# Optimization experiments

Hardware: AMD Instinct MI355X
Metric: run time of the kernel (lower is better)

The kernel has to match this reference:

```python
import jax, jax.numpy as jnp
import numpy as np

N = 100000      # nodes
E = 1600000     # edges (avg degree 16)
DIN = 64
DOUT = 64
C = 8           # num classes; label -1 means unknown


def _xavier(key, shape):
    a = jnp.sqrt(6.0 / (shape[0] + shape[1]))
    return jax.random.uniform(key, shape, jnp.float32, -a, a)


def setup_inputs():
    key = jax.random.key(0)
    ks = jax.random.split(key, 17)
    return {
        "x": jax.random.normal(ks[0], (N, DIN), jnp.float32),
        "adj_low_vals": jax.random.uniform(ks[1], (E,), jnp.float32) / 16.0,
        "adj_high_vals": jax.random.uniform(ks[2], (E,), jnp.float32) / 16.0,
        "weight_low": _xavier(ks[3], (DIN, DOUT)),
        "weight_high": _xavier(ks[4], (DIN, DOUT)),
        "weight_mlp": _xavier(ks[5], (DIN, DOUT)),
        "att_vec_low_fr": _xavier(ks[6], (DOUT, 1)),
        "att_vec_high_fr": _xavier(ks[7], (DOUT, 1)),
        "att_vec_low_be": _xavier(ks[8], (DOUT, 1)),
        "att_vec_high_be": _xavier(ks[9], (DOUT, 1)),
        "att_vec_low_unk": _xavier(ks[10], (DOUT, 1)),
        "att_vec_high_unk": _xavier(ks[11], (DOUT, 1)),
        "att_vec_mlp": _xavier(ks[12], (DOUT, 1)),
        "att_vec7": _xavier(ks[13], (7, 7)),
        "edge_src": jax.random.randint(ks[14], (E,), 0, N),
        "edge_dst": jax.random.randint(ks[15], (E,), 0, N),
        "label_unk": jax.random.randint(ks[16], (N,), -1, C),
    }


def reference(x, adj_low_vals, adj_high_vals, weight_low, weight_high, weight_mlp,
              att_vec_low_fr, att_vec_high_fr, att_vec_low_be, att_vec_high_be,
              att_vec_low_unk, att_vec_high_unk, att_vec_mlp, att_vec7,
              edge_src, edge_dst, label_unk):
    def spmm(vals, feats):  # out[dst] += vals * feats[src]  (sparse [N,N] @ [N,D])
        return jax.ops.segment_sum(vals[:, None] * feats[edge_src], edge_dst, num_segments=N)

    output_low = jax.nn.relu(spmm(adj_low_vals, x @ weight_low))
    output_high = jax.nn.relu(spmm(adj_high_vals, x @ weight_high))
    output_mlp = jax.nn.relu(x @ weight_mlp)

    # per-edge fake label: 2 if either endpoint unknown (<0), 1 if labels differ
    # (both known) -> heterophilous, else 0 -> homophilous
    sl = label_unk[edge_src]
    dl = label_unk[edge_dst]
    fake = jnp.where((sl < 0) | (dl < 0), 2, jnp.where(sl != dl, 1, 0))

    h_low_e = output_low[edge_src]    # [E, DOUT] gathered messages
    h_high_e = output_high[edge_src]

    def agg(h_e, k):  # masked segment-sum over destination nodes
        m = (fake == k).astype(h_e.dtype)[:, None]
        return jax.ops.segment_sum(h_e * m, edge_dst, num_segments=N)

    neigh_homo_low, neigh_hete_low, neigh_unk_low = agg(h_low_e, 0), agg(h_low_e, 1), agg(h_low_e, 2)
    neigh_homo_high, neigh_hete_high, neigh_unk_high = agg(h_high_e, 0), agg(h_high_e, 1), agg(h_high_e, 2)

    # attention7 (fr_high_g is None branch)
    feats = jax.nn.sigmoid(jnp.concatenate([
        neigh_hete_low @ att_vec_low_fr, neigh_hete_high @ att_vec_high_fr,
        neigh_homo_low @ att_vec_low_be, neigh_homo_high @ att_vec_high_be,
        neigh_unk_low @ att_vec_low_unk, neigh_unk_high @ att_vec_high_unk,
        output_mlp @ att_vec_mlp], axis=1))  # [N, 7]
    att = jax.nn.softmax((feats @ att_vec7) / 7.0, axis=1)

    return 7.0 * (att[:, 0:1] * neigh_hete_low + att[:, 1:2] * neigh_hete_high
                  + att[:, 2:3] * neigh_homo_low + att[:, 3:4] * neigh_homo_high
                  + att[:, 4:5] * neigh_unk_low + att[:, 5:6] * neigh_unk_high
                  + att[:, 6:7] * output_mlp)
```

## Files before the change

kernel.cpp:

```cpp
#include <hip/hip_runtime.h>
#include <hip/hip_bf16.h>

typedef unsigned int u32;
typedef unsigned short u16;
typedef unsigned long long u64;

typedef __attribute__((ext_vector_type(8))) short bf16x8;
typedef __attribute__((ext_vector_type(4))) float f32x4;

static __device__ __forceinline__ float bflo(u32 u) { return __uint_as_float(u << 16); }
static __device__ __forceinline__ float bfhi(u32 u) { return __uint_as_float(u & 0xFFFF0000u); }
static __device__ __forceinline__ float bf2f(u16 u) { return __uint_as_float((u32)u << 16); }
static __device__ __forceinline__ u32 f2bf(float f) {
    u32 u = __float_as_uint(f);
    return (u + 0x7FFFu + ((u >> 16) & 1u)) >> 16;
}
static __device__ __forceinline__ u32 packbf(float lo, float hi) {
    return f2bf(lo) | (f2bf(hi) << 16);
}
static __device__ __forceinline__ float ldf(const u16* p16, int idx, int isf32) {
    return isf32 ? ((const float*)p16)[idx] : bf2f(p16[idx]);
}
static __device__ __forceinline__ void load4(const u16* p, int q, int isf32, float* v) {
    if (isf32) {
        float4 t = ((const float4*)p)[q];
        v[0] = t.x; v[1] = t.y; v[2] = t.z; v[3] = t.w;
    } else {
        u32 a = ((const u32*)p)[q * 2], b = ((const u32*)p)[q * 2 + 1];
        v[0] = bflo(a); v[1] = bfhi(a); v[2] = bflo(b); v[3] = bfhi(b);
    }
}
static __device__ __forceinline__ float sanitize(float v, float code) {
    return (fabsf(v) < 1e30f) ? v : code;
}

static __device__ __forceinline__ float wave_sum(float v) {
#pragma unroll
    for (int o = 32; o; o >>= 1) v += __shfl_xor(v, o, 64);
    return v;
}
static __device__ __forceinline__ float group_sum(float v) {
#pragma unroll
    for (int o = 8; o; o >>= 1) v += __shfl_xor(v, o, 64);
    return v;
}


__global__ void k_sentinel(float* __restrict__ out, int n, float val) {
    int i = blockIdx.x * blockDim.x + threadIdx.x;
    if (i < n) out[i] = val;
}

__global__ void k_zero_sniff(int* __restrict__ p, int n, const u16* __restrict__ x,
                             int* __restrict__ flag) {
    int i = blockIdx.x * blockDim.x + threadIdx.x;
    if (i < n) p[i] = 0;
    if (blockIdx.x == 0 && threadIdx.x < 64) {
        int lane = threadIdx.x;
        int wild = 0;
        for (int k = 0; k < 64; k++) {
            u32 u = x[lane * 64 + k];
            int e = (u >> 7) & 0xFF;
            if (e < 96 || e > 135) wild++;
        }
        float tot = wave_sum((float)wild);
        if (lane == 0) *flag = (tot > 200.f) ? 1 : 0;
    }
}


__global__ void k_hist(const int* __restrict__ dst, int E, int* __restrict__ deg) {
    int i = blockIdx.x * blockDim.x + threadIdx.x;
    if (i < E) atomicAdd(&deg[dst[i]], 1);
}

__global__ void k_scan_partial(const int* __restrict__ deg, int n, int* __restrict__ bsum) {
    int t = threadIdx.x;
    int base = blockIdx.x * 1024 + t * 4;
    int s = 0;
#pragma unroll
    for (int j = 0; j < 4; j++) {
        int idx = base + j;
        if (idx < n) s += deg[idx];
    }
    __shared__ int sh[256];
    sh[t] = s;
    __syncthreads();
    for (int d = 128; d; d >>= 1) {
        if (t < d) sh[t] += sh[t + d];
        __syncthreads();
    }
    if (t == 0) bsum[blockIdx.x] = sh[0];
}

__global__ void k_scan_bsum(const int* __restrict__ bsum, int nb, int* __restrict__ boff) {
    int t = threadIdx.x;
    int v = (t < nb) ? bsum[t] : 0;
    __shared__ int sh[256];
    sh[t] = v;
    __syncthreads();
    for (int d = 1; d < 256; d <<= 1) {
        int u = (t >= d) ? sh[t - d] : 0;
        __syncthreads();
        sh[t] += u;
        __syncthreads();
    }
    if (t < nb) boff[t] = sh[t] - v;
}

__global__ void k_scan_final(const int* __restrict__ deg, int n, const int* __restrict__ boff,
                             int* __restrict__ offsets, int Etot) {
    int t = threadIdx.x;
    int base = blockIdx.x * 1024 + t * 4;
    int v[4];
    int s = 0;
#pragma unroll
    for (int j = 0; j < 4; j++) {
        int idx = base + j;
        v[j] = (idx < n) ? deg[idx] : 0;
        s += v[j];
    }
    __shared__ int sh[256];
    sh[t] = s;
    __syncthreads();
    for (int d = 1; d < 256; d <<= 1) {
        int u = (t >= d) ? sh[t - d] : 0;
        __syncthreads();
        sh[t] += u;
        __syncthreads();
    }
    int ex = sh[t] - s + boff[blockIdx.x];
#pragma unroll
    for (int j = 0; j < 4; j++) {
        int idx = base + j;
        if (idx < n) offsets[idx] = ex;
        ex += v[j];
    }
    if (blockIdx.x == 0 && t == 0) offsets[n] = Etot;
}

__global__ void k_scatter(const int* __restrict__ src, const int* __restrict__ dst,
                          const u16* __restrict__ avl, const u16* __restrict__ avh,
                          const int* __restrict__ lab, int E,
                          const int* __restrict__ offsets, int* __restrict__ cursor,
                          u64* __restrict__ epay, const int* __restrict__ flag) {
    int i = blockIdx.x * blockDim.x + threadIdx.x;
    if (i >= E) return;
    int isf32 = *flag;
    int d = dst[i];
    int pos = offsets[d] + atomicAdd(&cursor[d], 1);
    if ((unsigned)pos >= (unsigned)E) return;
    int s = src[i];
    int sl = lab[s], dl = lab[d];
    int fake = (sl < 0 || dl < 0) ? 2 : ((sl != dl) ? 1 : 0);
    u32 lo32 = (u32)(s | (fake << 20));
    u32 hi32 = isf32 ? packbf(((const float*)avl)[i], ((const float*)avh)[i])
                     : ((u32)avl[i] | ((u32)avh[i] << 16));
    epay[pos] = ((u64)hi32 << 32) | lo32;
}


__global__ void k_prepB(const u16* __restrict__ wl, const u16* __restrict__ wh,
                        const u16* __restrict__ wm, u16* __restrict__ Bpack,
                        const int* __restrict__ flag) {
    int isf32 = *flag;
    for (int idx = threadIdx.x; idx < 12 * 2 * 64; idx += 256) {
        int slot = idx >> 6;
        int ln = idx & 63;
        int ct = slot >> 1, c = slot & 1;
        int mat = ct >> 2;
        const u16* W = (mat == 0) ? wl : (mat == 1) ? wh : wm;
        int col = (ct & 3) * 16 + (ln & 15);
        int kbase = c * 32 + (ln >> 4) * 8;
        u16* dst = Bpack + (size_t)idx * 8;
#pragma unroll
        for (int j = 0; j < 8; j++) dst[j] = (u16)f2bf(ldf(W, (kbase + j) * 64 + col, isf32));
    }
}

__launch_bounds__(256) __global__
void k_gemm_mfma(const u16* __restrict__ x, const u16* __restrict__ Bpack, int N,
                 u32* __restrict__ xwlh, float* __restrict__ omlp,
                 const int* __restrict__ flag) {
    int isf32 = *flag;
    int lane = threadIdx.x & 63;
    int wv = (blockIdx.x * 256 + threadIdx.x) >> 6;
    int nw = gridDim.x * 4;
    int m = lane & 15, quad = lane >> 4;
    int ntiles = (N + 15) >> 4;
    for (int tile = wv; tile < ntiles; tile += nw) {
        int r0 = tile * 16;
        int arow = min(r0 + m, N - 1);
        bf16x8 a[2];
#pragma unroll
        for (int c = 0; c < 2; c++) {
            int base = arow * 64 + c * 32 + quad * 8;
            if (isf32) {
                const float* xf = (const float*)x;
#pragma unroll
                for (int j = 0; j < 8; j++) a[c][j] = (short)f2bf(xf[base + j]);
            } else {
#pragma unroll
                for (int j = 0; j < 8; j++) a[c][j] = (short)x[base + j];
            }
        }
        f32x4 acc[12];
#pragma unroll
        for (int t = 0; t < 12; t++) acc[t] = (f32x4){0.f, 0.f, 0.f, 0.f};
#pragma unroll
        for (int t = 0; t < 12; t++) {
#pragma unroll
            for (int c = 0; c < 2; c++) {
                bf16x8 b = *(const bf16x8*)(Bpack + (size_t)((t * 2 + c) * 64 + lane) * 8);
                acc[t] = __builtin_amdgcn_mfma_f32_16x16x32_bf16(a[c], b, acc[t], 0, 0, 0);
            }
        }
#pragma unroll
        for (int t = 0; t < 4; t++) {
#pragma unroll
            for (int r = 0; r < 4; r++) {
                int row = r0 + quad * 4 + r;
                if (row < N) {
                    int o = row * 64 + t * 16 + m;
                    xwlh[o] = packbf(acc[t][r], acc[t + 4][r]);
                    omlp[o] = fmaxf(acc[t + 8][r], 0.f);
                }
            }
        }
    }
}


__launch_bounds__(256) __global__
void k_spmm4n(const u32* __restrict__ xwlh, const u64* __restrict__ epay,
              const int* __restrict__ offsets, int N, int E, u32* __restrict__ outlh) {
    int lane = threadIdx.x & 63;
    int gwave = blockIdx.x * 4 + (threadIdx.x >> 6);
    int g = lane & 15, gi = lane >> 4;
    int node = gwave * 4 + gi;
    bool vn = node < N;
    int s = vn ? offsets[node] : 0;
    int e = vn ? offsets[node + 1] : 0;
    int deg = e - s;
    int md = deg;
    md = max(md, __shfl_xor(md, 16, 64));
    md = max(md, __shfl_xor(md, 32, 64));
    int Nm1 = N - 1, Em1 = E - 1;
    float aL[4] = {0.f, 0.f, 0.f, 0.f}, aH[4] = {0.f, 0.f, 0.f, 0.f};
    for (int t = 0; t < md; t += 2) {
#pragma unroll
        for (int u = 0; u < 2; u++) {
            int tt = t + u;
            int idx = min(max(s + min(tt, deg - 1), 0), Em1);
            u64 p = epay[idx];
            float w = (tt < deg) ? 1.f : 0.f;
            int sj = min((int)(p & 0xFFFFF), Nm1);
            u32 vv = (u32)(p >> 32);
            float vl = w * bflo(vv), vh = w * bfhi(vv);
            uint4 R = *((const uint4*)(xwlh + (size_t)sj * 64) + g);
            aL[0] += vl * bflo(R.x); aH[0] += vh * bfhi(R.x);
            aL[1] += vl * bflo(R.y); aH[1] += vh * bfhi(R.y);
            aL[2] += vl * bflo(R.z); aH[2] += vh * bfhi(R.z);
            aL[3] += vl * bflo(R.w); aH[3] += vh * bfhi(R.w);
        }
    }
    if (vn) {
        uint4 W;
        W.x = packbf(fmaxf(aL[0], 0.f), fmaxf(aH[0], 0.f));
        W.y = packbf(fmaxf(aL[1], 0.f), fmaxf(aH[1], 0.f));
        W.z = packbf(fmaxf(aL[2], 0.f), fmaxf(aH[2], 0.f));
        W.w = packbf(fmaxf(aL[3], 0.f), fmaxf(aH[3], 0.f));
        ((uint4*)(outlh + (size_t)node * 64))[g] = W;
    }
}


__launch_bounds__(256) __global__
void k_agg4n(const u32* __restrict__ outlh, const u64* __restrict__ epay,
             const int* __restrict__ offsets,
             const u16* __restrict__ aLF, const u16* __restrict__ aHF,
             const u16* __restrict__ aLB, const u16* __restrict__ aHB,
             const u16* __restrict__ aLU, const u16* __restrict__ aHU,
             const u16* __restrict__ aM, const u16* __restrict__ a7, int N, int E,
             float* __restrict__ out, const int* __restrict__ flag) {
    int isf32 = *flag;
    int lane = threadIdx.x & 63;
    int gwave = blockIdx.x * 4 + (threadIdx.x >> 6);
    int g = lane & 15, gi = lane >> 4;
    int node = gwave * 4 + gi;
    bool vn = node < N;
    int s = vn ? offsets[node] : 0;
    int e = vn ? offsets[node + 1] : 0;
    int deg = e - s;
    int md = deg;
    md = max(md, __shfl_xor(md, 16, 64));
    md = max(md, __shfl_xor(md, 32, 64));
    int Nm1 = N - 1, Em1 = E - 1;
    float heL[4] = {0, 0, 0, 0}, heH[4] = {0, 0, 0, 0};
    float hoL[4] = {0, 0, 0, 0}, hoH[4] = {0, 0, 0, 0};
    float unL[4] = {0, 0, 0, 0}, unH[4] = {0, 0, 0, 0};
    for (int t = 0; t < md; t += 2) {
#pragma unroll
        for (int u = 0; u < 2; u++) {
            int tt = t + u;
            int idx = min(max(s + min(tt, deg - 1), 0), Em1);
            u64 p = epay[idx];
            int fk = (int)(p >> 20) & 3;
            bool valid = (tt < deg);
            float whe = (valid && fk == 1) ? 1.f : 0.f;
            float who = (valid && fk == 0) ? 1.f : 0.f;
            float wun = (valid && fk == 2) ? 1.f : 0.f;
            int sj = min((int)(p & 0xFFFFF), Nm1);
            uint4 R = *((const uint4*)(outlh + (size_t)sj * 64) + g);
            float lo0 = bflo(R.x), hi0 = bfhi(R.x);
            float lo1 = bflo(R.y), hi1 = bfhi(R.y);
            float lo2 = bflo(R.z), hi2 = bfhi(R.z);
            float lo3 = bflo(R.w), hi3 = bfhi(R.w);
            heL[0] += whe * lo0; heH[0] += whe * hi0;
            heL[1] += whe * lo1; heH[1] += whe * hi1;
            heL[2] += whe * lo2; heH[2] += whe * hi2;
            heL[3] += whe * lo3; heH[3] += whe * hi3;
            hoL[0] += who * lo0; hoH[0] += who * hi0;
            hoL[1] += who * lo1; hoH[1] += who * hi1;
            hoL[2] += who * lo2; hoH[2] += who * hi2;
            hoL[3] += who * lo3; hoH[3] += who * hi3;
            unL[0] += wun * lo0; unH[0] += wun * hi0;
            unL[1] += wun * lo1; unH[1] += wun * hi1;
            unL[2] += wun * lo2; unH[2] += wun * hi2;
            unL[3] += wun * lo3; unH[3] += wun * hi3;
        }
    }
    float vLF[4], vHF[4], vLB[4], vHB[4], vLU[4], vHU[4], vM[4];
    load4(aLF, g, isf32, vLF);
    load4(aHF, g, isf32, vHF);
    load4(aLB, g, isf32, vLB);
    load4(aHB, g, isf32, vHB);
    load4(aLU, g, isf32, vLU);
    load4(aHU, g, isf32, vHU);
    load4(aM, g, isf32, vM);
    float mvv[4] = {0.f, 0.f, 0.f, 0.f};
    if (vn) {
        float4 MV = ((const float4*)(out + (size_t)node * 64))[g];
        mvv[0] = MV.x; mvv[1] = MV.y; mvv[2] = MV.z; mvv[3] = MV.w;
    }

    float p0 = 0, p1 = 0, p2 = 0, p3 = 0, p4 = 0, p5 = 0, p6 = 0;
#pragma unroll
    for (int k = 0; k < 4; k++) {
        p0 += heL[k] * vLF[k];
        p1 += heH[k] * vHF[k];
        p2 += hoL[k] * vLB[k];
        p3 += hoH[k] * vHB[k];
        p4 += unL[k] * vLU[k];
        p5 += unH[k] * vHU[k];
        p6 += mvv[k] * vM[k];
    }
    float d0 = group_sum(p0), d1 = group_sum(p1), d2 = group_sum(p2), d3 = group_sum(p3);
    float d4 = group_sum(p4), d5 = group_sum(p5), d6 = group_sum(p6);

    float f[7];
    f[0] = 1.f / (1.f + expf(-d0));
    f[1] = 1.f / (1.f + expf(-d1));
    f[2] = 1.f / (1.f + expf(-d2));
    f[3] = 1.f / (1.f + expf(-d3));
    f[4] = 1.f / (1.f + expf(-d4));
    f[5] = 1.f / (1.f + expf(-d5));
    f[6] = 1.f / (1.f + expf(-d6));

    float z[7];
#pragma unroll
    for (int jj = 0; jj < 7; jj++) {
        float acc = 0.f;
#pragma unroll
        for (int i = 0; i < 7; i++) acc += f[i] * ldf(a7, i * 7 + jj, isf32);
        z[jj] = acc * (1.f / 7.f);
    }
    float m = z[0];
#pragma unroll
    for (int jj = 1; jj < 7; jj++) m = fmaxf(m, z[jj]);
    float wsum = 0.f;
    float wv[7];
#pragma unroll
    for (int jj = 0; jj < 7; jj++) { wv[jj] = expf(z[jj] - m); wsum += wv[jj]; }
    float s7 = 7.f / wsum;

    if (vn) {
        float4 W;
        float o0 = wv[0] * heL[0] + wv[1] * heH[0] + wv[2] * hoL[0] + wv[3] * hoH[0] +
                   wv[4] * unL[0] + wv[5] * unH[0] + wv[6] * mvv[0];
        float o1 = wv[0] * heL[1] + wv[1] * heH[1] + wv[2] * hoL[1] + wv[3] * hoH[1] +
                   wv[4] * unL[1] + wv[5] * unH[1] + wv[6] * mvv[1];
        float o2 = wv[0] * heL[2] + wv[1] * heH[2] + wv[2] * hoL[2] + wv[3] * hoH[2] +
                   wv[4] * unL[2] + wv[5] * unH[2] + wv[6] * mvv[2];
        float o3 = wv[0] * heL[3] + wv[1] * heH[3] + wv[2] * hoL[3] + wv[3] * hoH[3] +
                   wv[4] * unL[3] + wv[5] * unH[3] + wv[6] * mvv[3];
        W.x = sanitize(o0 * s7, 333.f);
        W.y = sanitize(o1 * s7, 333.f);
        W.z = sanitize(o2 * s7, 333.f);
        W.w = sanitize(o3 * s7, 333.f);
        ((float4*)(out + (size_t)node * 64))[g] = W;
    }
}


extern "C" void kernel_launch(void* const* d_in, const int* in_sizes, int n_in, void* d_out,
                              int out_size, void* d_ws, size_t ws_size, hipStream_t stream) {
    const u16* x = (const u16*)d_in[0];
    const u16* avl = (const u16*)d_in[1];
    const u16* avh = (const u16*)d_in[2];
    const u16* wl = (const u16*)d_in[3];
    const u16* wh = (const u16*)d_in[4];
    const u16* wm = (const u16*)d_in[5];
    const u16* aLF = (const u16*)d_in[6];
    const u16* aHF = (const u16*)d_in[7];
    const u16* aLB = (const u16*)d_in[8];
    const u16* aHB = (const u16*)d_in[9];
    const u16* aLU = (const u16*)d_in[10];
    const u16* aHU = (const u16*)d_in[11];
    const u16* aM = (const u16*)d_in[12];
    const u16* a7 = (const u16*)d_in[13];
    const int* esrc = (const int*)d_in[14];
    const int* edst = (const int*)d_in[15];
    const int* lab = (const int*)d_in[16];
    float* out = (float*)d_out;

    const int N = in_sizes[0] / 64;
    const int E = in_sizes[1];

    char* w = (char*)d_ws;
    size_t off = 0;
    auto alloc = [&](size_t bytes) -> char* {
        char* p = w + off;
        off += (bytes + 255) & ~(size_t)255;
        return p;
    };
    int* flag = (int*)alloc(256);
    int* offsets = (int*)alloc((size_t)(N + 1) * 4);
    int* degcur = (int*)alloc((size_t)2 * N * 4);
    int* bsum = (int*)alloc(256 * 4);
    int* boff = (int*)alloc(256 * 4);
    u16* Bpack = (u16*)alloc(12 * 2 * 64 * 8 * 2);
    u64* epay = (u64*)alloc((size_t)E * 8);
    u32* xwlh = (u32*)alloc((size_t)N * 64 * 4);
    u32* outlh = (u32*)alloc((size_t)N * 64 * 4);

    if (ws_size < off) {
        k_sentinel<<<(out_size + 255) / 256, 256, 0, stream>>>(out, out_size, 1000.0f);
        return;
    }

    int* deg = degcur;
    int* cursor = degcur + N;
    int NB = (N + 1023) / 1024;

    k_zero_sniff<<<(2 * N + 255) / 256, 256, 0, stream>>>(degcur, 2 * N, x, flag);
    k_hist<<<(E + 255) / 256, 256, 0, stream>>>(edst, E, deg);
    k_scan_partial<<<NB, 256, 0, stream>>>(deg, N, bsum);
    k_scan_bsum<<<1, 256, 0, stream>>>(bsum, NB, boff);
    k_scan_final<<<NB, 256, 0, stream>>>(deg, N, boff, offsets, E);
    k_scatter<<<(E + 255) / 256, 256, 0, stream>>>(esrc, edst, avl, avh, lab, E, offsets, cursor,
                                                   epay, flag);

    k_prepB<<<1, 256, 0, stream>>>(wl, wh, wm, Bpack, flag);
    int ntiles = (N + 15) / 16;
    int gemmBlocks = (ntiles + 3) / 4;
    k_gemm_mfma<<<gemmBlocks, 256, 0, stream>>>(x, Bpack, N, xwlh, out , flag);

    int nodeBlocks = (N + 15) / 16;
    k_spmm4n<<<nodeBlocks, 256, 0, stream>>>(xwlh, epay, offsets, N, E, outlh);
    k_agg4n<<<nodeBlocks, 256, 0, stream>>>(outlh, epay, offsets, aLF, aHF, aLB, aHB, aLU, aHU,
                                            aM, a7, N, E, out, flag);
}
```

Measured before the change: 458.0 us.

## Split CSR edge scatter into two-pass bucketed scatter with LDS counters

```diff
diff --git a/kernel.cpp b/kernel.cpp
--- a/kernel.cpp
+++ b/kernel.cpp
@@ -139,24 +139,48 @@
     if (blockIdx.x == 0 && t == 0) offsets[n] = Etot;
 }
 
-__global__ void k_scatter(const int* __restrict__ src, const int* __restrict__ dst,
-                          const u16* __restrict__ avl, const u16* __restrict__ avh,
-                          const int* __restrict__ lab, int E,
-                          const int* __restrict__ offsets, int* __restrict__ cursor,
-                          u64* __restrict__ epay, const int* __restrict__ flag) {
+__global__ void k_scat1(const int* __restrict__ src, const int* __restrict__ dst,
+                        const u16* __restrict__ avl, const u16* __restrict__ avh,
+                        const int* __restrict__ lab, int E,
+                        const int* __restrict__ offsets, int* __restrict__ bcur,
+                        u64* __restrict__ etmp, const int* __restrict__ flag) {
     int i = blockIdx.x * blockDim.x + threadIdx.x;
     if (i >= E) return;
     int isf32 = *flag;
     int d = dst[i];
-    int pos = offsets[d] + atomicAdd(&cursor[d], 1);
+    int b = d >> 8;
+    int base = b << 8;
+    int rank = atomicAdd(&bcur[b * 16], 1);
+    int pos = offsets[base] + rank;
     if ((unsigned)pos >= (unsigned)E) return;
     int s = src[i];
     int sl = lab[s], dl = lab[d];
     int fake = (sl < 0 || dl < 0) ? 2 : ((sl != dl) ? 1 : 0);
-    u32 lo32 = (u32)(s | (fake << 20));
+    u32 lo32 = (u32)s | ((u32)fake << 20) | ((u32)(d - base) << 22);
     u32 hi32 = isf32 ? packbf(((const float*)avl)[i], ((const float*)avh)[i])
                      : ((u32)avl[i] | ((u32)avh[i] << 16));
-    epay[pos] = ((u64)hi32 << 32) | lo32;
+    etmp[pos] = ((u64)hi32 << 32) | lo32;
+}
+
+__launch_bounds__(256) __global__
+void k_scat2(const u64* __restrict__ etmp, const int* __restrict__ offsets, int N, int E,
+             u64* __restrict__ epay) {
+    __shared__ int cur[256];
+    int b = blockIdx.x;
+    int base = b << 8;
+    int t = threadIdx.x;
+    cur[t] = 0;
+    __syncthreads();
+    int hi = min(base + 256, N);
+    int r0 = offsets[base];
+    int r1 = offsets[hi];
+    for (int e = r0 + t; e < r1; e += 256) {
+        u64 p = etmp[e];
+        int dloc = (int)(p >> 22) & 0xFF;
+        int rank = atomicAdd(&cur[dloc], 1);
+        int pos = offsets[base + dloc] + rank;
+        if ((unsigned)pos < (unsigned)E) epay[pos] = p;
+    }
 }
 
 
@@ -245,13 +269,13 @@
     int md = deg;
     md = max(md, __shfl_xor(md, 16, 64));
     md = max(md, __shfl_xor(md, 32, 64));
-    int Nm1 = N - 1, Em1 = E - 1;
+    int Nm1 = N - 1;
     float aL[4] = {0.f, 0.f, 0.f, 0.f}, aH[4] = {0.f, 0.f, 0.f, 0.f};
     for (int t = 0; t < md; t += 2) {
 #pragma unroll
         for (int u = 0; u < 2; u++) {
             int tt = t + u;
-            int idx = min(max(s + min(tt, deg - 1), 0), Em1);
+            int idx = max(s + min(tt, deg - 1), 0);
             u64 p = epay[idx];
             float w = (tt < deg) ? 1.f : 0.f;
             int sj = min((int)(p & 0xFFFFF), Nm1);
@@ -295,7 +319,7 @@
     int md = deg;
     md = max(md, __shfl_xor(md, 16, 64));
     md = max(md, __shfl_xor(md, 32, 64));
-    int Nm1 = N - 1, Em1 = E - 1;
+    int Nm1 = N - 1;
     float heL[4] = {0, 0, 0, 0}, heH[4] = {0, 0, 0, 0};
     float hoL[4] = {0, 0, 0, 0}, hoH[4] = {0, 0, 0, 0};
     float unL[4] = {0, 0, 0, 0}, unH[4] = {0, 0, 0, 0};
@@ -303,7 +327,7 @@
 #pragma unroll
         for (int u = 0; u < 2; u++) {
             int tt = t + u;
-            int idx = min(max(s + min(tt, deg - 1), 0), Em1);
+            int idx = max(s + min(tt, deg - 1), 0);
             u64 p = epay[idx];
             int fk = (int)(p >> 20) & 3;
             bool valid = (tt < deg);
@@ -450,16 +474,19 @@
     }
 
     int* deg = degcur;
-    int* cursor = degcur + N;
+    int* bcur = degcur + N;
+    u64* etmp = (u64*)xwlh;
     int NB = (N + 1023) / 1024;
+    int NB2 = (N + 255) / 256;
 
     k_zero_sniff<<<(2 * N + 255) / 256, 256, 0, stream>>>(degcur, 2 * N, x, flag);
     k_hist<<<(E + 255) / 256, 256, 0, stream>>>(edst, E, deg);
     k_scan_partial<<<NB, 256, 0, stream>>>(deg, N, bsum);
     k_scan_bsum<<<1, 256, 0, stream>>>(bsum, NB, boff);
     k_scan_final<<<NB, 256, 0, stream>>>(deg, N, boff, offsets, E);
-    k_scatter<<<(E + 255) / 256, 256, 0, stream>>>(esrc, edst, avl, avh, lab, E, offsets, cursor,
-                                                   epay, flag);
+    k_scat1<<<(E + 255) / 256, 256, 0, stream>>>(esrc, edst, avl, avh, lab, E, offsets, bcur,
+                                                 etmp, flag);
+    k_scat2<<<NB2, 256, 0, stream>>>(etmp, offsets, N, E, epay);
 
     k_prepB<<<1, 256, 0, stream>>>(wl, wh, wm, Bpack, flag);
     int ntiles = (N + 15) / 16;
```

Result: slower. 484.7 us (+5.8%).
